# Performance work log

Measured on AMD Instinct MI355X. Metric: run time of the kernel, lower is better.

Reference implementation:

```python
import jax, jax.numpy as jnp
import numpy as np

B, T, D, H = 4096, 204800, 32, 64
EPS = 1e-10


def setup_inputs() -> dict:
    key = jax.random.key(0)
    ks = jax.random.split(key, 6)
    candidate = jax.random.normal(ks[0], (B, D), dtype=jnp.float32)
    behavior_values = jax.random.normal(ks[1], (T, D), dtype=jnp.float32)
    row_ids = jnp.sort(jax.random.randint(ks[2], (T,), 0, B, dtype=jnp.int32))
    in_dim = D + D + D * D  # concat of candidate, behavior, flattened outer product
    W1 = jax.random.normal(ks[3], (in_dim, H), dtype=jnp.float32) * (1.0 / np.sqrt(in_dim))
    b1 = jnp.zeros((H,), dtype=jnp.float32)
    alpha = jnp.zeros((H,), dtype=jnp.float32)  # Dice alpha init 0
    W2 = jax.random.normal(ks[4], (H, 1), dtype=jnp.float32) * (1.0 / np.sqrt(H))
    b2 = jnp.zeros((1,), dtype=jnp.float32)
    return {"candidate": candidate, "behavior_values": behavior_values,
            "row_ids": row_ids, "W1": W1, "b1": b1, "alpha": alpha,
            "W2": W2, "b2": b2}


def dice(x, alpha):
    mean = jnp.mean(x, axis=-1, keepdims=True)
    std = jnp.sqrt(jnp.mean(jnp.square(x - mean) + EPS, axis=-1, keepdims=True))
    p = jax.nn.sigmoid((x - mean) / (std + EPS))
    return alpha * (1.0 - p) * x + p * x


def reference(candidate, behavior_values, row_ids, W1, b1, alpha, W2, b2):
    # gather candidate embedding for each behavior row: [T, D]
    cand_per_behavior = candidate[row_ids]
    # outer product: behavior[:, :, None] * candidate[:, None, :] -> [T, D, D]
    outer = behavior_values[:, :, None] * cand_per_behavior[:, None, :]
    outer_flat = outer.reshape(outer.shape[0], D * D)  # [T, D*D]
    feat = jnp.concatenate([cand_per_behavior, behavior_values, outer_flat], axis=1)
    h = feat @ W1 + b1                 # [T, H]
    h = dice(h, alpha)
    w = h @ W2 + b2                    # [T, 1]
    weighted = behavior_values * w     # [T, D]
    out = jax.ops.segment_sum(weighted, row_ids, num_segments=B)  # [B, D]
    return out
```

## Files before the change

### kernel.cpp

```cpp
#include <hip/hip_runtime.h>
#include <cstddef>

#define DICE_EPS 1e-10f

typedef __attribute__((ext_vector_type(8))) short bf16x8;
typedef __attribute__((ext_vector_type(4))) float f32x4;
typedef __attribute__((ext_vector_type(4))) unsigned int u32x4;

__device__ inline void f2bf_split(float x, short& hi, short& lo) {
  const unsigned u = __float_as_uint(x);
  hi = (short)(u >> 16);
  const float rem = x - __uint_as_float(u & 0xffff0000u);
  lo = (short)(__float_as_uint(rem) >> 16);
}

__global__ __launch_bounds__(256) void precompute_Mfrag(
    const float* __restrict__ cand, const float* __restrict__ W1,
    const int* __restrict__ row_ids, unsigned short* __restrict__ Mhi,
    unsigned short* __restrict__ Mlo, int* __restrict__ seg, int T, int B) {
  {
    const int t = blockIdx.x * 256 + threadIdx.x;
    if (t < T) {
      const int b = row_ids[t];
      const int a = (t == 0) ? 0 : row_ids[t - 1];
      if (t == 0) seg[0] = 0;
      for (int r = a + 1; r <= b; r++) seg[r] = t;
      if (t == T - 1)
        for (int r = b + 1; r <= B; r++) seg[r] = T;
    }
  }

  const int lane = threadIdx.x & 63;
  const int wv = threadIdx.x >> 6;
  const int r0 = (blockIdx.x >> 2) * 16;
  const int z = blockIdx.x & 3;
  const int q = z * 4 + wv;
  const int c = lane & 15, g = lane >> 4;

  __shared__ __align__(16) unsigned short limg[2][16 * 4 * 16 * 8];

  bf16x8 Ahi, Alo;
  {
    const f32x4* ap =
        reinterpret_cast<const f32x4*>(cand + (size_t)(r0 + c) * 32 + 8 * g);
    const f32x4 a0 = ap[0], a1 = ap[1];
    const float av[8] = {a0.x, a0.y, a0.z, a0.w, a1.x, a1.y, a1.z, a1.w};
#pragma unroll
    for (int j = 0; j < 8; j++) {
      short h, l;
      f2bf_split(av[j], h, l);
      Ahi[j] = h; Alo[j] = l;
    }
  }

#pragma unroll
  for (int m = 0; m < 8; m++) {
    const int np = 8 * q + m;
    const int i = np >> 2;
    const int k = 16 * (np & 3) + c;
    const float* bp = W1 + (size_t)(64 + 32 * i + 8 * g) * 64 + k;
    bf16x8 Bhi, Blo;
#pragma unroll
    for (int jj = 0; jj < 8; jj++) {
      short h, l;
      f2bf_split(bp[(size_t)jj * 64], h, l);
      Bhi[jj] = h; Blo[jj] = l;
    }
    f32x4 Cz = {0.f, 0.f, 0.f, 0.f};
    Cz = __builtin_amdgcn_mfma_f32_16x16x32_bf16(Alo, Bhi, Cz, 0, 0, 0);
    Cz = __builtin_amdgcn_mfma_f32_16x16x32_bf16(Ahi, Blo, Cz, 0, 0, 0);
    Cz = __builtin_amdgcn_mfma_f32_16x16x32_bf16(Ahi, Bhi, Cz, 0, 0, 0);
    const float bias = W1[(size_t)(32 + i) * 64 + k];

    const int nn = np & 3;
    const int jj2 = (np >> 2) & 7;
#pragma unroll
    for (int p = 0; p < 4; p++) {
      const float v = Cz[p] + bias;
      const int rr = 4 * g + p;
      const int idx = ((rr * 4 + nn) * 16 + c) * 8 + jj2;
      short h, l;
      f2bf_split(v, h, l);
      limg[0][idx] = (unsigned short)h;
      limg[1][idx] = (unsigned short)l;
    }
  }
  __syncthreads();

  {
    const u32x4* src_h = reinterpret_cast<const u32x4*>(limg[0]);
    const u32x4* src_l = reinterpret_cast<const u32x4*>(limg[1]);
    u32x4* dst_h = reinterpret_cast<u32x4*>(Mhi);
    u32x4* dst_l = reinterpret_cast<u32x4*>(Mlo);
#pragma unroll
    for (int it = 0; it < 4; it++) {
      const int u = it * 256 + threadIdx.x;
      const size_t dst = (size_t)(r0 * 4 + (u >> 4)) * 64 + z * 16 + (u & 15);
      dst_h[dst] = src_h[u];
      dst_l[dst] = src_l[u];
    }
  }
}

__global__ __launch_bounds__(256) void attention_mfma(
    const float* __restrict__ cand, const float* __restrict__ behavior,
    const float* __restrict__ W1, const float* __restrict__ b1,
    const float* __restrict__ alpha, const float* __restrict__ W2,
    const float* __restrict__ b2, const unsigned short* __restrict__ Mhi,
    const unsigned short* __restrict__ Mlo, const int* __restrict__ seg,
    float* __restrict__ out) {
  const int lane = threadIdx.x & 63;
  const int wid = threadIdx.x >> 6;
  const int r = blockIdx.x * 4 + wid;
  const int c = lane & 15;
  const int g = lane >> 4;

  __shared__ float wlds[4][16];

  const int t0 = seg[r];
  const int t1 = seg[r + 1];

  bf16x8 Bhi[4], Blo[4];
  {
    const bf16x8* mh =
        reinterpret_cast<const bf16x8*>(Mhi) + (size_t)r * 4 * 64 + lane;
    const bf16x8* ml =
        reinterpret_cast<const bf16x8*>(Mlo) + (size_t)r * 4 * 64 + lane;
#pragma unroll
    for (int n = 0; n < 4; n++) {
      Bhi[n] = mh[(size_t)n * 64];
      Blo[n] = ml[(size_t)n * 64];
    }
  }

  float base_n[4], al_n[4], w2_n[4];
#pragma unroll
  for (int n = 0; n < 4; n++) {
    base_n[n] = b1[16 * n + c];
    al_n[n] = alpha[16 * n + c];
    w2_n[n] = W2[16 * n + c];
  }
  for (int d = 0; d < 32; d++) {
    const float cd = cand[(size_t)r * 32 + d];
#pragma unroll
    for (int n = 0; n < 4; n++)
      base_n[n] = fmaf(cd, W1[(size_t)d * 64 + 16 * n + c], base_n[n]);
  }
  const float b2v = b2[0];

  float acc[8];
#pragma unroll
  for (int jj = 0; jj < 8; jj++) acc[jj] = 0.f;

  for (int tb = t0; tb < t1; tb += 16) {
    const int trow = tb + c;
    f32x4 a0 = {0.f, 0.f, 0.f, 0.f}, a1 = {0.f, 0.f, 0.f, 0.f};
    if (trow < t1) {
      const f32x4* bp =
          reinterpret_cast<const f32x4*>(behavior + (size_t)trow * 32 + 8 * g);
      a0 = bp[0];
      a1 = bp[1];
    }
    bf16x8 Ahi, Alo;
    {
      const float av[8] = {a0.x, a0.y, a0.z, a0.w, a1.x, a1.y, a1.z, a1.w};
#pragma unroll
      for (int j = 0; j < 8; j++) {
        short h, l;
        f2bf_split(av[j], h, l);
        Ahi[j] = h; Alo[j] = l;
      }
    }

    f32x4 C[4];
#pragma unroll
    for (int n = 0; n < 4; n++) {
      f32x4 cz = {0.f, 0.f, 0.f, 0.f};
      cz = __builtin_amdgcn_mfma_f32_16x16x32_bf16(Alo, Bhi[n], cz, 0, 0, 0);
      cz = __builtin_amdgcn_mfma_f32_16x16x32_bf16(Ahi, Blo[n], cz, 0, 0, 0);
      cz = __builtin_amdgcn_mfma_f32_16x16x32_bf16(Ahi, Bhi[n], cz, 0, 0, 0);
      C[n] = cz;
    }

    float hm[4][4];
    float s[4], s2[4];
#pragma unroll
    for (int j = 0; j < 4; j++) {
      float ss = 0.f, qq = 0.f;
#pragma unroll
      for (int n = 0; n < 4; n++) {
        const float h = C[n][j] + base_n[n];
        hm[j][n] = h;
        ss += h;
        qq += h * h;
      }
      s[j] = ss;
      s2[j] = qq;
    }
#pragma unroll
    for (int off = 1; off < 16; off <<= 1) {
#pragma unroll
      for (int j = 0; j < 4; j++) {
        s[j] += __shfl_xor(s[j], off, 64);
        s2[j] += __shfl_xor(s2[j], off, 64);
      }
    }

    float wp[4];
#pragma unroll
    for (int j = 0; j < 4; j++) {
      const float mean = s[j] * (1.f / 64.f);
      const float var = fmaxf(s2[j] * (1.f / 64.f) - mean * mean, 0.f);
      const float stdv = sqrtf(var + DICE_EPS);
      const float inv = __builtin_amdgcn_rcpf(stdv + DICE_EPS);
      float w = 0.f;
#pragma unroll
      for (int n = 0; n < 4; n++) {
        const float h = hm[j][n];
        const float e = __expf((mean - h) * inv);
        const float p = __builtin_amdgcn_rcpf(1.f + e);
        const float hd = (al_n[n] + p * (1.f - al_n[n])) * h;
        w = fmaf(hd, w2_n[n], w);
      }
      wp[j] = w;
    }
#pragma unroll
    for (int off = 1; off < 16; off <<= 1) {
#pragma unroll
      for (int j = 0; j < 4; j++) wp[j] += __shfl_xor(wp[j], off, 64);
    }

    if (c == 0) wlds[wid][4 * g + 0] = wp[0] + b2v;
    if (c == 1) wlds[wid][4 * g + 1] = wp[1] + b2v;
    if (c == 2) wlds[wid][4 * g + 2] = wp[2] + b2v;
    if (c == 3) wlds[wid][4 * g + 3] = wp[3] + b2v;
    const float w = wlds[wid][c];

    acc[0] = fmaf(a0.x, w, acc[0]);
    acc[1] = fmaf(a0.y, w, acc[1]);
    acc[2] = fmaf(a0.z, w, acc[2]);
    acc[3] = fmaf(a0.w, w, acc[3]);
    acc[4] = fmaf(a1.x, w, acc[4]);
    acc[5] = fmaf(a1.y, w, acc[5]);
    acc[6] = fmaf(a1.z, w, acc[6]);
    acc[7] = fmaf(a1.w, w, acc[7]);
  }

#pragma unroll
  for (int off = 1; off < 16; off <<= 1) {
#pragma unroll
    for (int jj = 0; jj < 8; jj++) acc[jj] += __shfl_xor(acc[jj], off, 64);
  }
  if (c == 0) {
    f32x4 o0 = {acc[0], acc[1], acc[2], acc[3]};
    f32x4 o1 = {acc[4], acc[5], acc[6], acc[7]};
    f32x4* op = reinterpret_cast<f32x4*>(out + (size_t)r * 32 + 8 * g);
    op[0] = o0;
    op[1] = o1;
  }
}

extern "C" void kernel_launch(void* const* d_in, const int* in_sizes, int n_in,
                              void* d_out, int out_size, void* d_ws, size_t ws_size,
                              hipStream_t stream) {
  const float* cand     = (const float*)d_in[0];
  const float* behavior = (const float*)d_in[1];
  const int*   row_ids  = (const int*)d_in[2];
  const float* W1       = (const float*)d_in[3];
  const float* b1       = (const float*)d_in[4];
  const float* alpha    = (const float*)d_in[5];
  const float* W2       = (const float*)d_in[6];
  const float* b2       = (const float*)d_in[7];
  float* out = (float*)d_out;

  const int B = in_sizes[0] / 32;
  const int T = in_sizes[2];

  unsigned short* Mhi = (unsigned short*)d_ws;
  unsigned short* Mlo = Mhi + (size_t)B * 2048;
  int* seg = (int*)(Mlo + (size_t)B * 2048);

  const int nblk = max((B / 16) * 4, (T + 255) / 256);
  precompute_Mfrag<<<nblk, 256, 0, stream>>>(cand, W1, row_ids, Mhi, Mlo, seg,
                                             T, B);
  attention_mfma<<<B / 4, 256, 0, stream>>>(cand, behavior, W1, b1, alpha, W2,
                                            b2, Mhi, Mlo, seg, out);
}
```

Baseline: 116.1 us.

## Precompute candidate bias via MFMA, use DPP reductions, unroll tokens by two

The per-row base term (b1 + cand·W1[0:32]) moves into the precompute kernel, computed with split-bf16 MFMA and stored to a workspace buffer, so the scalar 32-step loop leaves the attention kernel. Cross-lane reductions switch from shfl_xor to DPP row ops, and the LDS broadcast of weights becomes a register select plus one shuffle. The token loop handles two 16-row tiles per iteration, the block size drops to 128 threads, and rsq replaces sqrt plus rcp. This adds workspace traffic and raises register pressure. The rsq form also drops the outer epsilon on std, a small numeric difference.

```diff
diff --git a/kernel.cpp b/kernel.cpp
--- a/kernel.cpp
+++ b/kernel.cpp
@@ -14,10 +14,22 @@
   lo = (short)(__float_as_uint(rem) >> 16);
 }
 
+#define DPP_ADD(v, ctrl)                                             \
+  ((v) + __int_as_float(__builtin_amdgcn_update_dpp(                 \
+             0, __float_as_int(v), (ctrl), 0xF, 0xF, true)))
+#define REDUCE16(v)            \
+  do {                         \
+    v = DPP_ADD(v, 0xB1);      \
+    v = DPP_ADD(v, 0x4E);      \
+    v = DPP_ADD(v, 0x128);     \
+    v = DPP_ADD(v, 0x124);     \
+  } while (0)
+
 __global__ __launch_bounds__(256) void precompute_Mfrag(
     const float* __restrict__ cand, const float* __restrict__ W1,
-    const int* __restrict__ row_ids, unsigned short* __restrict__ Mhi,
-    unsigned short* __restrict__ Mlo, int* __restrict__ seg, int T, int B) {
+    const float* __restrict__ b1, const int* __restrict__ row_ids,
+    unsigned short* __restrict__ Mhi, unsigned short* __restrict__ Mlo,
+    float* __restrict__ Base, int* __restrict__ seg, int T, int B) {
   {
     const int t = blockIdx.x * 256 + threadIdx.x;
     if (t < T) {
@@ -85,6 +97,26 @@
       limg[1][idx] = (unsigned short)l;
     }
   }
+
+  if (z == 0) {
+    const int k = 16 * wv + c;
+    const float* bp = W1 + (size_t)(8 * g) * 64 + k;
+    bf16x8 Bhi, Blo;
+#pragma unroll
+    for (int jj = 0; jj < 8; jj++) {
+      short h, l;
+      f2bf_split(bp[(size_t)jj * 64], h, l);
+      Bhi[jj] = h; Blo[jj] = l;
+    }
+    f32x4 Cz = {0.f, 0.f, 0.f, 0.f};
+    Cz = __builtin_amdgcn_mfma_f32_16x16x32_bf16(Alo, Bhi, Cz, 0, 0, 0);
+    Cz = __builtin_amdgcn_mfma_f32_16x16x32_bf16(Ahi, Blo, Cz, 0, 0, 0);
+    Cz = __builtin_amdgcn_mfma_f32_16x16x32_bf16(Ahi, Bhi, Cz, 0, 0, 0);
+    const float bias = b1[k];
+#pragma unroll
+    for (int p = 0; p < 4; p++)
+      Base[(size_t)(r0 + 4 * g + p) * 64 + k] = Cz[p] + bias;
+  }
   __syncthreads();
 
   {
@@ -102,20 +134,17 @@
   }
 }
 
-__global__ __launch_bounds__(256) void attention_mfma(
-    const float* __restrict__ cand, const float* __restrict__ behavior,
-    const float* __restrict__ W1, const float* __restrict__ b1,
-    const float* __restrict__ alpha, const float* __restrict__ W2,
-    const float* __restrict__ b2, const unsigned short* __restrict__ Mhi,
-    const unsigned short* __restrict__ Mlo, const int* __restrict__ seg,
-    float* __restrict__ out) {
+__global__ __launch_bounds__(128) void attention_mfma(
+    const float* __restrict__ behavior, const float* __restrict__ alpha,
+    const float* __restrict__ W2, const float* __restrict__ b2,
+    const unsigned short* __restrict__ Mhi,
+    const unsigned short* __restrict__ Mlo, const float* __restrict__ Base,
+    const int* __restrict__ seg, float* __restrict__ out) {
   const int lane = threadIdx.x & 63;
   const int wid = threadIdx.x >> 6;
-  const int r = blockIdx.x * 4 + wid;
+  const int r = blockIdx.x * 2 + wid;
   const int c = lane & 15;
   const int g = lane >> 4;
-
-  __shared__ float wlds[4][16];
 
   const int t0 = seg[r];
   const int t1 = seg[r + 1];
@@ -136,121 +165,120 @@
   float base_n[4], al_n[4], w2_n[4];
 #pragma unroll
   for (int n = 0; n < 4; n++) {
-    base_n[n] = b1[16 * n + c];
+    base_n[n] = Base[(size_t)r * 64 + 16 * n + c];
     al_n[n] = alpha[16 * n + c];
     w2_n[n] = W2[16 * n + c];
   }
-  for (int d = 0; d < 32; d++) {
-    const float cd = cand[(size_t)r * 32 + d];
-#pragma unroll
-    for (int n = 0; n < 4; n++)
-      base_n[n] = fmaf(cd, W1[(size_t)d * 64 + 16 * n + c], base_n[n]);
-  }
   const float b2v = b2[0];
+  const int wsrc = ((c >> 2) << 4) | (c & 3);
 
   float acc[8];
 #pragma unroll
   for (int jj = 0; jj < 8; jj++) acc[jj] = 0.f;
 
-  for (int tb = t0; tb < t1; tb += 16) {
-    const int trow = tb + c;
-    f32x4 a0 = {0.f, 0.f, 0.f, 0.f}, a1 = {0.f, 0.f, 0.f, 0.f};
-    if (trow < t1) {
-      const f32x4* bp =
-          reinterpret_cast<const f32x4*>(behavior + (size_t)trow * 32 + 8 * g);
-      a0 = bp[0];
-      a1 = bp[1];
-    }
-    bf16x8 Ahi, Alo;
-    {
-      const float av[8] = {a0.x, a0.y, a0.z, a0.w, a1.x, a1.y, a1.z, a1.w};
+  for (int tb = t0; tb < t1; tb += 32) {
+    f32x4 a0[2], a1[2];
+    bf16x8 Ahi[2], Alo[2];
+#pragma unroll
+    for (int u = 0; u < 2; u++) {
+      const int trow = tb + 16 * u + c;
+      f32x4 x0 = {0.f, 0.f, 0.f, 0.f}, x1 = {0.f, 0.f, 0.f, 0.f};
+      if (trow < t1) {
+        const f32x4* bp =
+            reinterpret_cast<const f32x4*>(behavior + (size_t)trow * 32 + 8 * g);
+        x0 = bp[0];
+        x1 = bp[1];
+      }
+      a0[u] = x0;
+      a1[u] = x1;
+      const float av[8] = {x0.x, x0.y, x0.z, x0.w, x1.x, x1.y, x1.z, x1.w};
 #pragma unroll
       for (int j = 0; j < 8; j++) {
         short h, l;
         f2bf_split(av[j], h, l);
-        Ahi[j] = h; Alo[j] = l;
-      }
-    }
-
-    f32x4 C[4];
-#pragma unroll
-    for (int n = 0; n < 4; n++) {
-      f32x4 cz = {0.f, 0.f, 0.f, 0.f};
-      cz = __builtin_amdgcn_mfma_f32_16x16x32_bf16(Alo, Bhi[n], cz, 0, 0, 0);
-      cz = __builtin_amdgcn_mfma_f32_16x16x32_bf16(Ahi, Blo[n], cz, 0, 0, 0);
-      cz = __builtin_amdgcn_mfma_f32_16x16x32_bf16(Ahi, Bhi[n], cz, 0, 0, 0);
-      C[n] = cz;
-    }
-
-    float hm[4][4];
-    float s[4], s2[4];
-#pragma unroll
-    for (int j = 0; j < 4; j++) {
-      float ss = 0.f, qq = 0.f;
+        Ahi[u][j] = h; Alo[u][j] = l;
+      }
+    }
+
+    f32x4 C[2][4];
+#pragma unroll
+    for (int u = 0; u < 2; u++)
 #pragma unroll
       for (int n = 0; n < 4; n++) {
-        const float h = C[n][j] + base_n[n];
-        hm[j][n] = h;
-        ss += h;
-        qq += h * h;
-      }
-      s[j] = ss;
-      s2[j] = qq;
-    }
-#pragma unroll
-    for (int off = 1; off < 16; off <<= 1) {
+        f32x4 cz = {0.f, 0.f, 0.f, 0.f};
+        cz = __builtin_amdgcn_mfma_f32_16x16x32_bf16(Alo[u], Bhi[n], cz, 0, 0, 0);
+        cz = __builtin_amdgcn_mfma_f32_16x16x32_bf16(Ahi[u], Blo[n], cz, 0, 0, 0);
+        cz = __builtin_amdgcn_mfma_f32_16x16x32_bf16(Ahi[u], Bhi[n], cz, 0, 0, 0);
+        C[u][n] = cz;
+      }
+
+    float s[2][4], s2[2][4];
+#pragma unroll
+    for (int u = 0; u < 2; u++)
 #pragma unroll
       for (int j = 0; j < 4; j++) {
-        s[j] += __shfl_xor(s[j], off, 64);
-        s2[j] += __shfl_xor(s2[j], off, 64);
-      }
-    }
-
-    float wp[4];
-#pragma unroll
-    for (int j = 0; j < 4; j++) {
-      const float mean = s[j] * (1.f / 64.f);
-      const float var = fmaxf(s2[j] * (1.f / 64.f) - mean * mean, 0.f);
-      const float stdv = sqrtf(var + DICE_EPS);
-      const float inv = __builtin_amdgcn_rcpf(stdv + DICE_EPS);
-      float w = 0.f;
-#pragma unroll
-      for (int n = 0; n < 4; n++) {
-        const float h = hm[j][n];
-        const float e = __expf((mean - h) * inv);
-        const float p = __builtin_amdgcn_rcpf(1.f + e);
-        const float hd = (al_n[n] + p * (1.f - al_n[n])) * h;
-        w = fmaf(hd, w2_n[n], w);
-      }
-      wp[j] = w;
-    }
-#pragma unroll
-    for (int off = 1; off < 16; off <<= 1) {
-#pragma unroll
-      for (int j = 0; j < 4; j++) wp[j] += __shfl_xor(wp[j], off, 64);
-    }
-
-    if (c == 0) wlds[wid][4 * g + 0] = wp[0] + b2v;
-    if (c == 1) wlds[wid][4 * g + 1] = wp[1] + b2v;
-    if (c == 2) wlds[wid][4 * g + 2] = wp[2] + b2v;
-    if (c == 3) wlds[wid][4 * g + 3] = wp[3] + b2v;
-    const float w = wlds[wid][c];
-
-    acc[0] = fmaf(a0.x, w, acc[0]);
-    acc[1] = fmaf(a0.y, w, acc[1]);
-    acc[2] = fmaf(a0.z, w, acc[2]);
-    acc[3] = fmaf(a0.w, w, acc[3]);
-    acc[4] = fmaf(a1.x, w, acc[4]);
-    acc[5] = fmaf(a1.y, w, acc[5]);
-    acc[6] = fmaf(a1.z, w, acc[6]);
-    acc[7] = fmaf(a1.w, w, acc[7]);
-  }
-
-#pragma unroll
-  for (int off = 1; off < 16; off <<= 1) {
-#pragma unroll
-    for (int jj = 0; jj < 8; jj++) acc[jj] += __shfl_xor(acc[jj], off, 64);
-  }
+        float ss = 0.f, qq = 0.f;
+#pragma unroll
+        for (int n = 0; n < 4; n++) {
+          const float h = C[u][n][j] + base_n[n];
+          C[u][n][j] = h;
+          ss += h;
+          qq += h * h;
+        }
+        s[u][j] = ss;
+        s2[u][j] = qq;
+      }
+#pragma unroll
+    for (int u = 0; u < 2; u++)
+#pragma unroll
+      for (int j = 0; j < 4; j++) {
+        REDUCE16(s[u][j]);
+        REDUCE16(s2[u][j]);
+      }
+
+    float wp[2][4];
+#pragma unroll
+    for (int u = 0; u < 2; u++)
+#pragma unroll
+      for (int j = 0; j < 4; j++) {
+        const float mean = s[u][j] * (1.f / 64.f);
+        const float var = fmaxf(s2[u][j] * (1.f / 64.f) - mean * mean, 0.f);
+        const float inv = __builtin_amdgcn_rsqf(var + DICE_EPS);
+        float w = 0.f;
+#pragma unroll
+        for (int n = 0; n < 4; n++) {
+          const float h = C[u][n][j];
+          const float e = __expf((mean - h) * inv);
+          const float p = __builtin_amdgcn_rcpf(1.f + e);
+          const float hd = (al_n[n] + p * (1.f - al_n[n])) * h;
+          w = fmaf(hd, w2_n[n], w);
+        }
+        wp[u][j] = w;
+      }
+#pragma unroll
+    for (int u = 0; u < 2; u++)
+#pragma unroll
+      for (int j = 0; j < 4; j++) REDUCE16(wp[u][j]);
+
+#pragma unroll
+    for (int u = 0; u < 2; u++) {
+      const float t01 = (c & 1) ? wp[u][1] : wp[u][0];
+      const float t23 = (c & 1) ? wp[u][3] : wp[u][2];
+      const float vsel = (c & 2) ? t23 : t01;
+      const float w = __shfl(vsel, wsrc, 64) + b2v;
+      acc[0] = fmaf(a0[u].x, w, acc[0]);
+      acc[1] = fmaf(a0[u].y, w, acc[1]);
+      acc[2] = fmaf(a0[u].z, w, acc[2]);
+      acc[3] = fmaf(a0[u].w, w, acc[3]);
+      acc[4] = fmaf(a1[u].x, w, acc[4]);
+      acc[5] = fmaf(a1[u].y, w, acc[5]);
+      acc[6] = fmaf(a1[u].z, w, acc[6]);
+      acc[7] = fmaf(a1[u].w, w, acc[7]);
+    }
+  }
+
+#pragma unroll
+  for (int jj = 0; jj < 8; jj++) REDUCE16(acc[jj]);
   if (c == 0) {
     f32x4 o0 = {acc[0], acc[1], acc[2], acc[3]};
     f32x4 o1 = {acc[4], acc[5], acc[6], acc[7]};
@@ -278,11 +306,12 @@
 
   unsigned short* Mhi = (unsigned short*)d_ws;
   unsigned short* Mlo = Mhi + (size_t)B * 2048;
-  int* seg = (int*)(Mlo + (size_t)B * 2048);
+  float* Base = (float*)(Mlo + (size_t)B * 2048);
+  int* seg = (int*)(Base + (size_t)B * 64);
 
   const int nblk = max((B / 16) * 4, (T + 255) / 256);
-  precompute_Mfrag<<<nblk, 256, 0, stream>>>(cand, W1, row_ids, Mhi, Mlo, seg,
-                                             T, B);
-  attention_mfma<<<B / 4, 256, 0, stream>>>(cand, behavior, W1, b1, alpha, W2,
-                                            b2, Mhi, Mlo, seg, out);
+  precompute_Mfrag<<<nblk, 256, 0, stream>>>(cand, W1, b1, row_ids, Mhi, Mlo,
+                                             Base, seg, T, B);
+  attention_mfma<<<B / 2, 128, 0, stream>>>(behavior, alpha, W2, b2, Mhi, Mlo,
+                                            Base, seg, out);
 }
```

Result: slower. 118.9 us (+2.4%).
